# Kernel tuning notes

Hardware: AMD Instinct MI355X
Metric: run time of the kernel (lower is better)

## Reference

```python
import jax, jax.numpy as jnp
import numpy as np

SYM_LIST = jnp.array([0, 7, 12, 20], dtype=jnp.int32)
B, N = 128, 1000


def setup_inputs() -> dict:
    key = jax.random.key(0)
    k1, k2, k3, k4, k5 = jax.random.split(key, 5)
    return {
        "pred_r": jax.random.normal(k1, (B, 3, 3), dtype=jnp.float32),
        "pred_t": jax.random.normal(k2, (B, 1, 3), dtype=jnp.float32),
        "targets": jax.random.normal(k3, (B, N, 3), dtype=jnp.float32),
        "model_points": jax.random.normal(k4, (B, N, 3), dtype=jnp.float32),
        "idxs": jax.random.randint(k5, (B,), 0, 21, dtype=jnp.int32),
    }


def reference(pred_r, pred_t, targets, model_points, idxs):
    # rigid transform: model_points @ pred_r^T + pred_t  -> [B, N, 3]
    pred_points = jnp.einsum("bni,bji->bnj", model_points, pred_r) + pred_t

    # batched nearest-neighbor search (cdist + argmin), vectorized over batch
    # squared distances [B, N, N]: d2[b,i,j] = ||pred[b,i] - tgt[b,j]||^2
    p2 = jnp.sum(pred_points * pred_points, axis=-1, keepdims=True)      # [B,N,1]
    t2 = jnp.sum(targets * targets, axis=-1, keepdims=True)             # [B,N,1]
    d2 = p2 + jnp.swapaxes(t2, 1, 2) - 2.0 * jnp.einsum(
        "bnd,bmd->bnm", pred_points, targets)
    inds = jnp.argmin(d2, axis=-1)                                       # [B,N]

    # gather nearest targets; apply only for symmetric object ids
    tgt_knn = jnp.take_along_axis(targets, inds[..., None], axis=1)      # [B,N,3]
    is_sym = jnp.isin(idxs, SYM_LIST)                                    # [B]
    tgt = jnp.where(is_sym[:, None, None], tgt_knn, targets)

    # mean over points of L2 norm, then mean over batch -> scalar
    dis = jnp.mean(jnp.linalg.norm(pred_points - tgt, axis=2), axis=1).mean()
    return dis
```

## Files before the change

### kernel.cpp

```cpp
#include <hip/hip_runtime.h>
#include <float.h>


#define BATCH 128
#define NPTS  1000
#define SPLIT 16
#define PTS_PER_BLK 64
#define LANES_PER_PT 8
#define JCHUNK (NPTS / LANES_PER_PT)
#define THREADS 512
#define NBLK (BATCH * SPLIT)

__global__ __launch_bounds__(THREADS) void pose_loss_kernel(
    const float* __restrict__ pred_r,
    const float* __restrict__ pred_t,
    const float* __restrict__ targets,
    const float* __restrict__ model_points,
    const int*   __restrict__ idxs,
    float* __restrict__ partial)
{
    const int b   = blockIdx.x / SPLIT;
    const int s   = blockIdx.x % SPLIT;
    const int tid = threadIdx.x;

    const int id = idxs[b];
    const bool sym = (id == 0) | (id == 7) | (id == 12) | (id == 20);

    const float* Rb = pred_r + b * 9;
    const float* Tb = pred_t + b * 3;
    const float R00 = Rb[0], R01 = Rb[1], R02 = Rb[2];
    const float R10 = Rb[3], R11 = Rb[4], R12 = Rb[5];
    const float R20 = Rb[6], R21 = Rb[7], R22 = Rb[8];
    const float T0 = Tb[0], T1 = Tb[1], T2 = Tb[2];

    __shared__ float tsh[3 * NPTS];
    if (sym) {
        const float4* tb4 =
            reinterpret_cast<const float4*>(targets + (size_t)b * 3 * NPTS);
        float4* tsh4 = reinterpret_cast<float4*>(tsh);
        #pragma unroll
        for (int k = tid; k < (3 * NPTS) / 4; k += THREADS)
            tsh4[k] = tb4[k];
        __syncthreads();
    }

    const int iloc = tid >> 3;
    const int sub  = tid & 7;
    const int i    = s * PTS_PER_BLK + iloc;

    float acc = 0.0f;
    if (i < NPTS) {
        const float* mp = model_points + ((size_t)b * NPTS + i) * 3;
        const float m0 = mp[0], m1 = mp[1], m2 = mp[2];
        const float px = fmaf(m0, R00, fmaf(m1, R01, fmaf(m2, R02, T0)));
        const float py = fmaf(m0, R10, fmaf(m1, R11, fmaf(m2, R12, T1)));
        const float pz = fmaf(m0, R20, fmaf(m1, R21, fmaf(m2, R22, T2)));

        if (sym) {
            float bestd = FLT_MAX;
            int   bestj = sub * JCHUNK;
            const int j0 = sub * JCHUNK;
            #pragma unroll 5
            for (int j = j0; j < j0 + JCHUNK; ++j) {
                const float dx = px - tsh[3 * j + 0];
                const float dy = py - tsh[3 * j + 1];
                const float dz = pz - tsh[3 * j + 2];
                const float d2 = fmaf(dx, dx, fmaf(dy, dy, dz * dz));
                if (d2 < bestd) { bestd = d2; bestj = j; }
            }
            #pragma unroll
            for (int off = 1; off < LANES_PER_PT; off <<= 1) {
                const float od = __shfl_xor(bestd, off, 64);
                const int   oj = __shfl_xor(bestj, off, 64);
                if (od < bestd || (od == bestd && oj < bestj)) {
                    bestd = od; bestj = oj;
                }
            }
            if (sub == 0) acc = sqrtf(bestd);
        } else if (sub == 0) {
            const float* tg = targets + ((size_t)b * NPTS + i) * 3;
            const float dx = px - tg[0], dy = py - tg[1], dz = pz - tg[2];
            acc = sqrtf(fmaf(dx, dx, fmaf(dy, dy, dz * dz)));
        }
    }

    #pragma unroll
    for (int off = 32; off > 0; off >>= 1)
        acc += __shfl_down(acc, off, 64);

    __shared__ float wsum[THREADS / 64];
    const int wid = tid >> 6, lane = tid & 63;
    if (lane == 0) wsum[wid] = acc;
    __syncthreads();
    if (tid == 0) {
        float s2 = 0.0f;
        #pragma unroll
        for (int w = 0; w < THREADS / 64; ++w) s2 += wsum[w];
        partial[blockIdx.x] = s2;
    }
}

__global__ __launch_bounds__(256) void pose_loss_reduce(
    const float* __restrict__ partial,
    float* __restrict__ out)
{
    const int tid = threadIdx.x;
    const float4* p4 = reinterpret_cast<const float4*>(partial);
    float acc = 0.0f;
    #pragma unroll
    for (int k = tid; k < NBLK / 4; k += 256) {
        const float4 v = p4[k];
        acc += (v.x + v.y) + (v.z + v.w);
    }

    #pragma unroll
    for (int off = 32; off > 0; off >>= 1)
        acc += __shfl_down(acc, off, 64);

    __shared__ float wsum[4];
    const int wid = tid >> 6, lane = tid & 63;
    if (lane == 0) wsum[wid] = acc;
    __syncthreads();
    if (tid == 0) {
        float s2 = (wsum[0] + wsum[1]) + (wsum[2] + wsum[3]);
        out[0] = s2 * (1.0f / (BATCH * NPTS));
    }
}

extern "C" void kernel_launch(void* const* d_in, const int* in_sizes, int n_in,
                              void* d_out, int out_size, void* d_ws, size_t ws_size,
                              hipStream_t stream) {
    const float* pred_r       = (const float*)d_in[0];
    const float* pred_t       = (const float*)d_in[1];
    const float* targets      = (const float*)d_in[2];
    const float* model_points = (const float*)d_in[3];
    const int*   idxs         = (const int*)d_in[4];
    float* out     = (float*)d_out;
    float* partial = (float*)d_ws;

    pose_loss_kernel<<<NBLK, THREADS, 0, stream>>>(
        pred_r, pred_t, targets, model_points, idxs, partial);
    pose_loss_reduce<<<1, 256, 0, stream>>>(partial, out);
}
```

Measured before the change: 80.70 us.

## Use SoA shared targets with packed float2 min-distance search

Targets are transposed into a structure-of-arrays layout in shared memory, so each lane reads x, y and z as packed float2 pairs and can use packed FP32 math. The argmin index tracking is dropped: since the loss only needs the nearest distance, a running fminf is enough. Lanes per point go from 8 to 4 and the grid is halved, giving each lane more work per block and fewer blocks. The risks are bank conflicts on the strided scatter into shared memory and lower occupancy from the smaller grid.

```diff
diff --git a/kernel.cpp b/kernel.cpp
--- a/kernel.cpp
+++ b/kernel.cpp
@@ -4,12 +4,15 @@
 
 #define BATCH 128
 #define NPTS  1000
-#define SPLIT 16
-#define PTS_PER_BLK 64
-#define LANES_PER_PT 8
-#define JCHUNK (NPTS / LANES_PER_PT)
+#define SPLIT 8
+#define PTS_PER_BLK 128
+#define LANES_PER_PT 4
+#define NPAIR (NPTS / 2)
+#define PCHUNK (NPAIR / LANES_PER_PT)
 #define THREADS 512
 #define NBLK (BATCH * SPLIT)
+
+typedef float f32x2 __attribute__((ext_vector_type(2)));
 
 __global__ __launch_bounds__(THREADS) void pose_loss_kernel(
     const float* __restrict__ pred_r,
@@ -37,51 +40,56 @@
     if (sym) {
         const float4* tb4 =
             reinterpret_cast<const float4*>(targets + (size_t)b * 3 * NPTS);
-        float4* tsh4 = reinterpret_cast<float4*>(tsh);
-        #pragma unroll
-        for (int k = tid; k < (3 * NPTS) / 4; k += THREADS)
-            tsh4[k] = tb4[k];
+        for (int k = tid; k < (3 * NPTS) / 4; k += THREADS) {
+            const float4 v = tb4[k];
+            const int f = 4 * k;
+            tsh[((f + 0) % 3) * NPTS + (f + 0) / 3] = v.x;
+            tsh[((f + 1) % 3) * NPTS + (f + 1) / 3] = v.y;
+            tsh[((f + 2) % 3) * NPTS + (f + 2) / 3] = v.z;
+            tsh[((f + 3) % 3) * NPTS + (f + 3) / 3] = v.w;
+        }
         __syncthreads();
     }
 
-    const int iloc = tid >> 3;
-    const int sub  = tid & 7;
+    const int iloc = tid >> 2;
+    const int sub  = tid & 3;
     const int i    = s * PTS_PER_BLK + iloc;
+    const bool valid = (i < NPTS);
+
+    float m0 = 0.f, m1 = 0.f, m2 = 0.f;
+    if (valid) {
+        const float* mp = model_points + ((size_t)b * NPTS + i) * 3;
+        m0 = mp[0]; m1 = mp[1]; m2 = mp[2];
+    }
+    const float px = fmaf(m0, R00, fmaf(m1, R01, fmaf(m2, R02, T0)));
+    const float py = fmaf(m0, R10, fmaf(m1, R11, fmaf(m2, R12, T1)));
+    const float pz = fmaf(m0, R20, fmaf(m1, R21, fmaf(m2, R22, T2)));
 
     float acc = 0.0f;
-    if (i < NPTS) {
-        const float* mp = model_points + ((size_t)b * NPTS + i) * 3;
-        const float m0 = mp[0], m1 = mp[1], m2 = mp[2];
-        const float px = fmaf(m0, R00, fmaf(m1, R01, fmaf(m2, R02, T0)));
-        const float py = fmaf(m0, R10, fmaf(m1, R11, fmaf(m2, R12, T1)));
-        const float pz = fmaf(m0, R20, fmaf(m1, R21, fmaf(m2, R22, T2)));
-
-        if (sym) {
-            float bestd = FLT_MAX;
-            int   bestj = sub * JCHUNK;
-            const int j0 = sub * JCHUNK;
-            #pragma unroll 5
-            for (int j = j0; j < j0 + JCHUNK; ++j) {
-                const float dx = px - tsh[3 * j + 0];
-                const float dy = py - tsh[3 * j + 1];
-                const float dz = pz - tsh[3 * j + 2];
-                const float d2 = fmaf(dx, dx, fmaf(dy, dy, dz * dz));
-                if (d2 < bestd) { bestd = d2; bestj = j; }
-            }
-            #pragma unroll
-            for (int off = 1; off < LANES_PER_PT; off <<= 1) {
-                const float od = __shfl_xor(bestd, off, 64);
-                const int   oj = __shfl_xor(bestj, off, 64);
-                if (od < bestd || (od == bestd && oj < bestj)) {
-                    bestd = od; bestj = oj;
-                }
-            }
-            if (sub == 0) acc = sqrtf(bestd);
-        } else if (sub == 0) {
-            const float* tg = targets + ((size_t)b * NPTS + i) * 3;
-            const float dx = px - tg[0], dy = py - tg[1], dz = pz - tg[2];
-            acc = sqrtf(fmaf(dx, dx, fmaf(dy, dy, dz * dz)));
+    if (sym) {
+        const f32x2* tx2 = reinterpret_cast<const f32x2*>(tsh);
+        const f32x2* ty2 = reinterpret_cast<const f32x2*>(tsh + NPTS);
+        const f32x2* tz2 = reinterpret_cast<const f32x2*>(tsh + 2 * NPTS);
+        const f32x2 px2 = {px, px}, py2 = {py, py}, pz2 = {pz, pz};
+        f32x2 bd = {FLT_MAX, FLT_MAX};
+        const int k0 = sub * PCHUNK;
+        #pragma unroll 5
+        for (int k = k0; k < k0 + PCHUNK; ++k) {
+            const f32x2 dx = px2 - tx2[k];
+            const f32x2 dy = py2 - ty2[k];
+            const f32x2 dz = pz2 - tz2[k];
+            const f32x2 d2 = dx * dx + dy * dy + dz * dz;
+            bd.x = fminf(bd.x, d2.x);
+            bd.y = fminf(bd.y, d2.y);
         }
+        float best = fminf(bd.x, bd.y);
+        best = fminf(best, __shfl_xor(best, 1, 64));
+        best = fminf(best, __shfl_xor(best, 2, 64));
+        if (sub == 0 && valid) acc = sqrtf(best);
+    } else if (sub == 0 && valid) {
+        const float* tg = targets + ((size_t)b * NPTS + i) * 3;
+        const float dx = px - tg[0], dy = py - tg[1], dz = pz - tg[2];
+        acc = sqrtf(fmaf(dx, dx, fmaf(dy, dy, dz * dz)));
     }
 
     #pragma unroll
```

Measured after the change: 80.50 us. About the same (-0.3%).
